# Kernel tuning notes

Measured on AMD Instinct MI355X. Metric: run time of the kernel, lower is better.

The kernel has to match this reference:

```python
import jax, jax.numpy as jnp
import numpy as np

N_USERS = 100_000
N_ENTITIES = 400_000
N_NODES = N_USERS + N_ENTITIES  # 500k
DIM = 64
N_EDGES = 2_000_000
BATCH = 4096
N_LAYERS = 3
CF_WEIGHT = 1.0
L2_REG = 1e-4


def setup_inputs() -> dict:
    key = jax.random.key(0)
    k_emb, k_e, k_u, k_p, k_n = jax.random.split(key, 5)
    # xavier_uniform on (N, D): bound = sqrt(6/(N+D))
    bound = float(np.sqrt(6.0 / (N_NODES + DIM)))
    emb = jax.random.uniform(k_emb, (N_NODES, DIM), jnp.float32, -bound, bound)
    edge_index = jax.random.randint(k_e, (2, N_EDGES), 0, N_NODES, dtype=jnp.int32)
    user_idx = jax.random.randint(k_u, (BATCH,), 0, N_USERS, dtype=jnp.int32)
    pos_item = jax.random.randint(k_p, (BATCH,), 0, N_NODES, dtype=jnp.int32)
    neg_item = jax.random.randint(k_n, (BATCH,), 0, N_NODES, dtype=jnp.int32)
    return {"emb": emb, "edge_index": edge_index, "user_idx": user_idx,
            "pos_item": pos_item, "neg_item": neg_item}


def _lightgcn(emb, edge_index, n_layers):
    # LGConv(normalize=True): x' = D^{-1/2} A D^{-1/2} x, no self loops.
    n = emb.shape[0]
    src, dst = edge_index[0], edge_index[1]
    deg = jax.ops.segment_sum(jnp.ones_like(dst, dtype=emb.dtype), dst,
                              num_segments=n)
    dinv = jnp.where(deg > 0, jax.lax.rsqrt(jnp.maximum(deg, 1e-12)), 0.0)
    norm = dinv[src] * dinv[dst]  # [E]
    x = emb
    acc = emb  # layer-0 term of the mean over stacked layers
    for _ in range(n_layers):
        msgs = x[src] * norm[:, None]  # [E, D] gather + scale
        x = jax.ops.segment_sum(msgs, dst, num_segments=n)  # scatter-add
        acc = acc + x
    return acc / (n_layers + 1)  # mean over (layers+1) stacked embeddings


def reference(emb, edge_index, user_idx, pos_item, neg_item):
    all_layer = _lightgcn(emb, edge_index, N_LAYERS)
    u = all_layer[user_idx]
    p = all_layer[pos_item]
    n_ = all_layer[neg_item]
    pos_score = jnp.sum(u * p, axis=-1)
    neg_score = jnp.sum(u * n_, axis=-1)
    # BPRLoss: -mean(logsigmoid(pos - neg)) == mean(softplus(neg - pos))
    cf_loss = jnp.mean(jax.nn.softplus(neg_score - pos_score))
    u_ego = emb[user_idx]
    p_ego = emb[pos_item]
    n_ego = emb[neg_item]
    reg_loss = 0.5 * (jnp.sum(u_ego ** 2) + jnp.sum(p_ego ** 2)
                      + jnp.sum(n_ego ** 2)) / float(BATCH)
    return CF_WEIGHT * cf_loss + L2_REG * reg_loss
```

## Files before the change

### kernel.cpp

```cpp
#include <hip/hip_runtime.h>
#include <cstdint>
#include <cstddef>

#define N_USERS   100000
#define N_NODES   500000
#define DIM       64
#define N_EDGES   2000000
#define BATCH     4096
#define SCAN_B    1024
#define NBLK      ((N_NODES + SCAN_B - 1) / SCAN_B)
#define X1C_CAP   350000
#define LA_CAP    150000
#define EDG4_BLK  ((N_EDGES / 4 + 255) / 256)
#define CONV_BLK  ((N_NODES * 16 + 255) / 256)
#define PROP_BLK  2048

typedef unsigned char uchar;
typedef unsigned short ushort;
typedef unsigned int uint;

__device__ __forceinline__ ushort f2bf(float f) {
    uint u = __float_as_uint(f);
    uint r = u + 0x7FFFu + ((u >> 16) & 1u);
    return (ushort)(r >> 16);
}
__device__ __forceinline__ float bflo(uint u) { return __uint_as_float(u << 16); }
__device__ __forceinline__ float bfhi(uint u) { return __uint_as_float(u & 0xFFFF0000u); }

__global__ void k_mark(const int* __restrict__ u, const int* __restrict__ p,
                       const int* __restrict__ n, uchar* __restrict__ f3,
                       uchar* __restrict__ fA, uchar* __restrict__ fB) {
    int i = blockIdx.x * blockDim.x + threadIdx.x;
    if (i >= 3 * BATCH) return;
    int idx;
    if (i < BATCH)          idx = u[i];
    else if (i < 2 * BATCH) idx = p[i - BATCH];
    else                    idx = n[i - 2 * BATCH];
    f3[idx] = 1; fA[idx] = 1; fB[idx] = 1;
}

__global__ void k_degconv(const int* __restrict__ src, const int* __restrict__ dst,
                          int* __restrict__ deg, const uchar* __restrict__ f3,
                          uchar* __restrict__ fA,
                          const float* __restrict__ emb, ushort* __restrict__ embs) {
    if (blockIdx.x < EDG4_BLK) {
        int t = blockIdx.x * blockDim.x + threadIdx.x;
        if (t < N_EDGES / 4) {
            int4 s0 = ((const int4*)src)[t];
            int4 d0 = ((const int4*)dst)[t];
            atomicAdd(&deg[d0.x], 1); atomicAdd(&deg[d0.y], 1);
            atomicAdd(&deg[d0.z], 1); atomicAdd(&deg[d0.w], 1);
            if (f3[d0.x] && !fA[s0.x]) fA[s0.x] = 1;
            if (f3[d0.y] && !fA[s0.y]) fA[s0.y] = 1;
            if (f3[d0.z] && !fA[s0.z]) fA[s0.z] = 1;
            if (f3[d0.w] && !fA[s0.w]) fA[s0.w] = 1;
        }
    } else {
        int c = (blockIdx.x - EDG4_BLK) * blockDim.x + threadIdx.x;
        if (c < N_NODES * 16) {
            float4 v = ((const float4*)emb)[c];
            uint2 o;
            o.x = (uint)f2bf(v.x) | ((uint)f2bf(v.y) << 16);
            o.y = (uint)f2bf(v.z) | ((uint)f2bf(v.w) << 16);
            ((uint2*)embs)[c] = o;
        }
    }
}

__global__ void k_expand(const int* __restrict__ src, const int* __restrict__ dst,
                         const uchar* __restrict__ fin, uchar* __restrict__ fout) {
    int t = blockIdx.x * blockDim.x + threadIdx.x;
    if (t < N_EDGES / 4) {
        int4 s0 = ((const int4*)src)[t];
        int4 d0 = ((const int4*)dst)[t];
        if (fin[d0.x] && !fout[s0.x]) fout[s0.x] = 1;
        if (fin[d0.y] && !fout[s0.y]) fout[s0.y] = 1;
        if (fin[d0.z] && !fout[s0.z]) fout[s0.z] = 1;
        if (fin[d0.w] && !fout[s0.w]) fout[s0.w] = 1;
    }
}

__global__ void k_scanA(const int* __restrict__ deg, const uchar* __restrict__ fA,
                        const uchar* __restrict__ fB, int* __restrict__ bsumD,
                        int* __restrict__ bsumP) {
    __shared__ int sD[SCAN_B];
    __shared__ int sP[SCAN_B];
    int i = blockIdx.x * SCAN_B + threadIdx.x;
    int d = 0, pk = 0;
    if (i < N_NODES) { d = deg[i]; pk = (int)fA[i] | ((int)fB[i] << 16); }
    sD[threadIdx.x] = d; sP[threadIdx.x] = pk;
    __syncthreads();
    for (int off = SCAN_B / 2; off; off >>= 1) {
        if (threadIdx.x < off) {
            sD[threadIdx.x] += sD[threadIdx.x + off];
            sP[threadIdx.x] += sP[threadIdx.x + off];
        }
        __syncthreads();
    }
    if (threadIdx.x == 0) { bsumD[blockIdx.x] = sD[0]; bsumP[blockIdx.x] = sP[0]; }
}

__global__ void k_scanB(const int* __restrict__ bsumD, const int* __restrict__ bsumP,
                        int* __restrict__ boffD, int* __restrict__ boffA,
                        int* __restrict__ boffB, int* __restrict__ counts) {
    __shared__ int sD[512];
    __shared__ int sA[512];
    __shared__ int sB[512];
    int d = (threadIdx.x < NBLK) ? bsumD[threadIdx.x] : 0;
    int p = (threadIdx.x < NBLK) ? bsumP[threadIdx.x] : 0;
    int a = p & 0xFFFF, b = p >> 16;
    sD[threadIdx.x] = d; sA[threadIdx.x] = a; sB[threadIdx.x] = b;
    __syncthreads();
    for (int off = 1; off < 512; off <<= 1) {
        int tD = (threadIdx.x >= off) ? sD[threadIdx.x - off] : 0;
        int tA = (threadIdx.x >= off) ? sA[threadIdx.x - off] : 0;
        int tB = (threadIdx.x >= off) ? sB[threadIdx.x - off] : 0;
        __syncthreads();
        sD[threadIdx.x] += tD; sA[threadIdx.x] += tA; sB[threadIdx.x] += tB;
        __syncthreads();
    }
    if (threadIdx.x < NBLK) {
        boffD[threadIdx.x] = sD[threadIdx.x] - d;
        boffA[threadIdx.x] = sA[threadIdx.x] - a;
        boffB[threadIdx.x] = sB[threadIdx.x] - b;
    }
    if (threadIdx.x == 511) { counts[0] = sA[511]; counts[1] = sB[511]; }
}

__global__ void k_scanC(const int* __restrict__ deg, const uchar* __restrict__ fA,
                        const uchar* __restrict__ fB,
                        const int* __restrict__ boffD, const int* __restrict__ boffA,
                        const int* __restrict__ boffB,
                        int* __restrict__ rowstart, float* __restrict__ dinv,
                        int* __restrict__ mapA, int* __restrict__ mapB,
                        int4* __restrict__ listA4, int4* __restrict__ listB4) {
    __shared__ int sD[SCAN_B];
    __shared__ int sP[SCAN_B];
    int i = blockIdx.x * SCAN_B + threadIdx.x;
    int d = 0, a = 0, b = 0;
    if (i < N_NODES) { d = deg[i]; a = (int)fA[i]; b = (int)fB[i]; }
    sD[threadIdx.x] = d; sP[threadIdx.x] = a | (b << 16);
    __syncthreads();
    for (int off = 1; off < SCAN_B; off <<= 1) {
        int tD = (threadIdx.x >= off) ? sD[threadIdx.x - off] : 0;
        int tP = (threadIdx.x >= off) ? sP[threadIdx.x - off] : 0;
        __syncthreads();
        sD[threadIdx.x] += tD; sP[threadIdx.x] += tP;
        __syncthreads();
    }
    if (i < N_NODES) {
        int exD = sD[threadIdx.x] - d + boffD[blockIdx.x];
        int incP = sP[threadIdx.x];
        int exA = (incP & 0xFFFF) - a + boffA[blockIdx.x];
        int exB = (incP >> 16) - b + boffB[blockIdx.x];
        rowstart[i] = exD;
        float dv = (d > 0) ? rsqrtf((float)d) : 0.0f;
        dinv[i] = dv;
        mapA[i] = a ? exA : -1;
        mapB[i] = b ? exB : -1;
        int4 ent = make_int4(exD, exD + d, __float_as_int(dv), 0);
        if (a) listA4[exA] = ent;
        if (b) listB4[exB] = ent;
    }
}

__global__ void k_scatter(const int* __restrict__ src, const int* __restrict__ dst,
                          const uchar* __restrict__ fB, int* __restrict__ rowstart,
                          int* __restrict__ csr_src) {
    int t = blockIdx.x * blockDim.x + threadIdx.x;
    if (t < N_EDGES / 4) {
        int4 s0 = ((const int4*)src)[t];
        int4 d0 = ((const int4*)dst)[t];
        if (fB[d0.x]) csr_src[atomicAdd(&rowstart[d0.x], 1)] = s0.x;
        if (fB[d0.y]) csr_src[atomicAdd(&rowstart[d0.y], 1)] = s0.y;
        if (fB[d0.z]) csr_src[atomicAdd(&rowstart[d0.z], 1)] = s0.z;
        if (fB[d0.w]) csr_src[atomicAdd(&rowstart[d0.w], 1)] = s0.w;
    }
}

__global__ void k_prop1(const ushort* __restrict__ embs, const int4* __restrict__ listB4,
                        const int* __restrict__ counts, const int* __restrict__ csr_src,
                        const float* __restrict__ dinv, ushort* __restrict__ x1c) {
    int lane = threadIdx.x & 63;
    int sub = lane >> 4, q = lane & 15;
    int wv = (blockIdx.x * blockDim.x + threadIdx.x) >> 6;
    int nw = (gridDim.x * blockDim.x) >> 6;
    int cnt = counts[1];
    for (; wv < cnt; wv += nw) {
        int4 nb = listB4[wv];
        float4 acc = {0.f, 0.f, 0.f, 0.f};
        for (int i = nb.x + sub; i < nb.y; i += 4) {
            int s = csr_src[i];
            float dvs = dinv[s];
            uint2 u = *(const uint2*)(embs + (size_t)s * DIM + q * 4);
            acc.x = fmaf(bflo(u.x), dvs, acc.x);
            acc.y = fmaf(bfhi(u.x), dvs, acc.y);
            acc.z = fmaf(bflo(u.y), dvs, acc.z);
            acc.w = fmaf(bfhi(u.y), dvs, acc.w);
        }
        for (int off = 16; off <= 32; off <<= 1) {
            acc.x += __shfl_xor(acc.x, off, 64);
            acc.y += __shfl_xor(acc.y, off, 64);
            acc.z += __shfl_xor(acc.z, off, 64);
            acc.w += __shfl_xor(acc.w, off, 64);
        }
        if (sub == 0) {
            float dv = __int_as_float(nb.z);
            float d2 = dv * dv;
            uint2 o;
            o.x = (uint)f2bf(acc.x * d2) | ((uint)f2bf(acc.y * d2) << 16);
            o.y = (uint)f2bf(acc.z * d2) | ((uint)f2bf(acc.w * d2) << 16);
            *(uint2*)(x1c + (size_t)wv * DIM + q * 4) = o;
        }
    }
}

__global__ void k_prop2(const ushort* __restrict__ x1c, const int* __restrict__ mapB,
                        const int4* __restrict__ listA4, const int* __restrict__ counts,
                        const int* __restrict__ csr_src, ushort* __restrict__ x2c) {
    int lane = threadIdx.x & 63;
    int sub = lane >> 4, q = lane & 15;
    int wv = (blockIdx.x * blockDim.x + threadIdx.x) >> 6;
    int nw = (gridDim.x * blockDim.x) >> 6;
    int cnt = counts[0];
    for (; wv < cnt; wv += nw) {
        int4 nb = listA4[wv];
        float4 acc = {0.f, 0.f, 0.f, 0.f};
        for (int i = nb.x + sub; i < nb.y; i += 4) {
            int s = csr_src[i];
            int slot = mapB[s];
            uint2 u = *(const uint2*)(x1c + (size_t)slot * DIM + q * 4);
            acc.x += bflo(u.x); acc.y += bfhi(u.x);
            acc.z += bflo(u.y); acc.w += bfhi(u.y);
        }
        for (int off = 16; off <= 32; off <<= 1) {
            acc.x += __shfl_xor(acc.x, off, 64);
            acc.y += __shfl_xor(acc.y, off, 64);
            acc.z += __shfl_xor(acc.z, off, 64);
            acc.w += __shfl_xor(acc.w, off, 64);
        }
        if (sub == 0) {
            float dv = __int_as_float(nb.z);
            float d2 = dv * dv;
            uint2 o;
            o.x = (uint)f2bf(acc.x * d2) | ((uint)f2bf(acc.y * d2) << 16);
            o.y = (uint)f2bf(acc.z * d2) | ((uint)f2bf(acc.w * d2) << 16);
            *(uint2*)(x2c + (size_t)wv * DIM + q * 4) = o;
        }
    }
}

__device__ __forceinline__ float x3_row(const ushort* __restrict__ x2c,
                                        const int* __restrict__ mapA,
                                        const int* __restrict__ csr_src,
                                        const int4* __restrict__ listB4,
                                        const int* __restrict__ mapB,
                                        int t, int lane) {
    int4 nb = listB4[mapB[t]];
    float acc = 0.f;
    for (int i = nb.x; i < nb.y; ++i) {
        int s = csr_src[i];
        int slot = mapA[s];
        acc += __uint_as_float((uint)x2c[(size_t)slot * DIM + lane] << 16);
    }
    return acc * __int_as_float(nb.z);
}

__global__ void k_loss(const float* __restrict__ emb, const ushort* __restrict__ x1c,
                       const ushort* __restrict__ x2c,
                       const int* __restrict__ mapA, const int* __restrict__ mapB,
                       const int4* __restrict__ listB4, const int* __restrict__ csr_src,
                       const float* __restrict__ dinv,
                       const int* __restrict__ u, const int* __restrict__ p,
                       const int* __restrict__ n, float* __restrict__ out) {
    int lane = threadIdx.x & 63;
    int w = (blockIdx.x * blockDim.x + threadIdx.x) >> 6;
    if (w >= BATCH) return;
    int ui = u[w], pi = p[w], ni = n[w];
    float dvu = dinv[ui], dvp = dinv[pi], dvn = dinv[ni];
    float rdu = dvu > 0.f ? 1.f / dvu : 0.f;
    float rdp = dvp > 0.f ? 1.f / dvp : 0.f;
    float rdn = dvn > 0.f ? 1.f / dvn : 0.f;
    float ue = emb[(size_t)ui * DIM + lane];
    float pe = emb[(size_t)pi * DIM + lane];
    float ne = emb[(size_t)ni * DIM + lane];
    float u1 = __uint_as_float((uint)x1c[(size_t)mapB[ui] * DIM + lane] << 16) * rdu;
    float p1 = __uint_as_float((uint)x1c[(size_t)mapB[pi] * DIM + lane] << 16) * rdp;
    float n1 = __uint_as_float((uint)x1c[(size_t)mapB[ni] * DIM + lane] << 16) * rdn;
    float u2 = __uint_as_float((uint)x2c[(size_t)mapA[ui] * DIM + lane] << 16) * rdu;
    float p2 = __uint_as_float((uint)x2c[(size_t)mapA[pi] * DIM + lane] << 16) * rdp;
    float n2 = __uint_as_float((uint)x2c[(size_t)mapA[ni] * DIM + lane] << 16) * rdn;
    float u3 = x3_row(x2c, mapA, csr_src, listB4, mapB, ui, lane);
    float p3 = x3_row(x2c, mapA, csr_src, listB4, mapB, pi, lane);
    float n3 = x3_row(x2c, mapA, csr_src, listB4, mapB, ni, lane);
    float uall = 0.25f * (ue + u1 + u2 + u3);
    float pall = 0.25f * (pe + p1 + p2 + p3);
    float nall = 0.25f * (ne + n1 + n2 + n3);
    float pos = uall * pall;
    float neg = uall * nall;
    float sq  = ue * ue + pe * pe + ne * ne;
    for (int off = 32; off; off >>= 1) {
        pos += __shfl_xor(pos, off, 64);
        neg += __shfl_xor(neg, off, 64);
        sq  += __shfl_xor(sq,  off, 64);
    }
    if (lane == 0) {
        float z = neg - pos;
        float sp = fmaxf(z, 0.0f) + log1pf(expf(-fabsf(z)));
        float contrib = sp * (1.0f / BATCH) + 1e-4f * 0.5f * sq * (1.0f / BATCH);
        atomicAdd(out, contrib);
    }
}

extern "C" void kernel_launch(void* const* d_in, const int* in_sizes, int n_in,
                              void* d_out, int out_size, void* d_ws, size_t ws_size,
                              hipStream_t stream) {
    const float* emb  = (const float*)d_in[0];
    const int*   edge = (const int*)d_in[1];
    const int*   src  = edge;
    const int*   dst  = edge + N_EDGES;
    const int*   uidx = (const int*)d_in[2];
    const int*   pidx = (const int*)d_in[3];
    const int*   nidx = (const int*)d_in[4];
    float* out = (float*)d_out;

    char* w = (char*)d_ws;
    ushort* embs    = (ushort*)w;                w += (size_t)N_NODES * DIM * 2;
    ushort* x1c     = (ushort*)w;                w += (size_t)X1C_CAP * DIM * 2;
    ushort* x2c     = (ushort*)w;                w += (size_t)LA_CAP * DIM * 2;
    float*  dinv    = (float*)w;                 w += (size_t)N_NODES * 4;
    int*    rowstart= (int*)w;                   w += (size_t)N_NODES * 4;
    int*    csr_src = (int*)w;                   w += (size_t)N_EDGES * 4;
    int*    mapA    = (int*)w;                   w += (size_t)N_NODES * 4;
    int*    mapB    = (int*)w;                   w += (size_t)N_NODES * 4;
    int4*   listA4  = (int4*)w;                  w += (size_t)LA_CAP * 16;
    int4*   listB4  = (int4*)w;                  w += (size_t)X1C_CAP * 16;
    char*   zbase   = w;
    int*    deg     = (int*)w;                   w += (size_t)N_NODES * 4;
    uchar*  flags   = (uchar*)w;                 w += (size_t)3 * N_NODES;
    uchar*  f3 = flags;
    uchar*  fA = flags + N_NODES;
    uchar*  fB = flags + 2 * N_NODES;
    size_t  zbytes  = (size_t)(w - zbase);
    int*    bsumD   = (int*)w;                   w += (size_t)NBLK * 4;
    int*    boffD   = (int*)w;                   w += (size_t)NBLK * 4;
    int*    bsumP   = (int*)w;                   w += (size_t)NBLK * 4;
    int*    boffA   = (int*)w;                   w += (size_t)NBLK * 4;
    int*    boffB   = (int*)w;                   w += (size_t)NBLK * 4;
    int*    counts  = (int*)w;                   w += 16;

    hipMemsetAsync(zbase, 0, zbytes, stream);
    hipMemsetAsync(out, 0, 4, stream);

    k_mark<<<(3 * BATCH + 255) / 256, 256, 0, stream>>>(uidx, pidx, nidx, f3, fA, fB);

    k_degconv<<<EDG4_BLK + CONV_BLK, 256, 0, stream>>>(src, dst, deg, f3, fA,
                                                       emb, embs);

    k_expand<<<EDG4_BLK, 256, 0, stream>>>(src, dst, fA, fB);

    k_scanA<<<NBLK, SCAN_B, 0, stream>>>(deg, fA, fB, bsumD, bsumP);
    k_scanB<<<1, 512, 0, stream>>>(bsumD, bsumP, boffD, boffA, boffB, counts);
    k_scanC<<<NBLK, SCAN_B, 0, stream>>>(deg, fA, fB, boffD, boffA, boffB,
                                         rowstart, dinv, mapA, mapB, listA4, listB4);

    k_scatter<<<EDG4_BLK, 256, 0, stream>>>(src, dst, fB, rowstart, csr_src);

    k_prop1<<<PROP_BLK, 256, 0, stream>>>(embs, listB4, counts, csr_src, dinv, x1c);
    k_prop2<<<PROP_BLK, 256, 0, stream>>>(x1c, mapB, listA4, counts, csr_src, x2c);

    k_loss<<<(BATCH * 64 + 255) / 256, 256, 0, stream>>>(
        emb, x1c, x2c, mapA, mapB, listB4, csr_src, dinv, uidx, pidx, nidx, out);
}
```

Before: 470.7 us.

## Privatize degree histogram per XCD and move bf16 conversion into scatter kernel

```diff
diff --git a/kernel.cpp b/kernel.cpp
--- a/kernel.cpp
+++ b/kernel.cpp
@@ -9,8 +9,9 @@
 #define BATCH     4096
 #define SCAN_B    1024
 #define NBLK      ((N_NODES + SCAN_B - 1) / SCAN_B)
-#define X1C_CAP   350000
-#define LA_CAP    150000
+#define X1C_CAP   280000
+#define LA_CAP    100000
+#define NXCD      8
 #define EDG4_BLK  ((N_EDGES / 4 + 255) / 256)
 #define CONV_BLK  ((N_NODES * 16 + 255) / 256)
 #define PROP_BLK  2048
@@ -26,6 +27,12 @@
 }
 __device__ __forceinline__ float bflo(uint u) { return __uint_as_float(u << 16); }
 __device__ __forceinline__ float bfhi(uint u) { return __uint_as_float(u & 0xFFFF0000u); }
+
+__device__ __forceinline__ uint xcc_id() {
+    uint x;
+    asm volatile("s_getreg_b32 %0, hwreg(HW_REG_XCC_ID)" : "=s"(x));
+    return x & (NXCD - 1);
+}
 
 __global__ void k_mark(const int* __restrict__ u, const int* __restrict__ p,
                        const int* __restrict__ n, uchar* __restrict__ f3,
@@ -39,31 +46,22 @@
     f3[idx] = 1; fA[idx] = 1; fB[idx] = 1;
 }
 
-__global__ void k_degconv(const int* __restrict__ src, const int* __restrict__ dst,
-                          int* __restrict__ deg, const uchar* __restrict__ f3,
-                          uchar* __restrict__ fA,
-                          const float* __restrict__ emb, ushort* __restrict__ embs) {
-    if (blockIdx.x < EDG4_BLK) {
-        int t = blockIdx.x * blockDim.x + threadIdx.x;
-        if (t < N_EDGES / 4) {
-            int4 s0 = ((const int4*)src)[t];
-            int4 d0 = ((const int4*)dst)[t];
-            atomicAdd(&deg[d0.x], 1); atomicAdd(&deg[d0.y], 1);
-            atomicAdd(&deg[d0.z], 1); atomicAdd(&deg[d0.w], 1);
-            if (f3[d0.x] && !fA[s0.x]) fA[s0.x] = 1;
-            if (f3[d0.y] && !fA[s0.y]) fA[s0.y] = 1;
-            if (f3[d0.z] && !fA[s0.z]) fA[s0.z] = 1;
-            if (f3[d0.w] && !fA[s0.w]) fA[s0.w] = 1;
-        }
-    } else {
-        int c = (blockIdx.x - EDG4_BLK) * blockDim.x + threadIdx.x;
-        if (c < N_NODES * 16) {
-            float4 v = ((const float4*)emb)[c];
-            uint2 o;
-            o.x = (uint)f2bf(v.x) | ((uint)f2bf(v.y) << 16);
-            o.y = (uint)f2bf(v.z) | ((uint)f2bf(v.w) << 16);
-            ((uint2*)embs)[c] = o;
-        }
+__global__ void k_deghist(const int* __restrict__ src, const int* __restrict__ dst,
+                          int* __restrict__ degp, const uchar* __restrict__ f3,
+                          uchar* __restrict__ fA) {
+    int* mydeg = degp + (size_t)xcc_id() * N_NODES;
+    int t = blockIdx.x * blockDim.x + threadIdx.x;
+    if (t < N_EDGES / 4) {
+        int4 s0 = ((const int4*)src)[t];
+        int4 d0 = ((const int4*)dst)[t];
+        __hip_atomic_fetch_add(&mydeg[d0.x], 1, __ATOMIC_RELAXED, __HIP_MEMORY_SCOPE_WORKGROUP);
+        __hip_atomic_fetch_add(&mydeg[d0.y], 1, __ATOMIC_RELAXED, __HIP_MEMORY_SCOPE_WORKGROUP);
+        __hip_atomic_fetch_add(&mydeg[d0.z], 1, __ATOMIC_RELAXED, __HIP_MEMORY_SCOPE_WORKGROUP);
+        __hip_atomic_fetch_add(&mydeg[d0.w], 1, __ATOMIC_RELAXED, __HIP_MEMORY_SCOPE_WORKGROUP);
+        if (f3[d0.x] && !fA[s0.x]) fA[s0.x] = 1;
+        if (f3[d0.y] && !fA[s0.y]) fA[s0.y] = 1;
+        if (f3[d0.z] && !fA[s0.z]) fA[s0.z] = 1;
+        if (f3[d0.w] && !fA[s0.w]) fA[s0.w] = 1;
     }
 }
 
@@ -80,14 +78,19 @@
     }
 }
 
-__global__ void k_scanA(const int* __restrict__ deg, const uchar* __restrict__ fA,
-                        const uchar* __restrict__ fB, int* __restrict__ bsumD,
-                        int* __restrict__ bsumP) {
+__global__ void k_scanA(const int* __restrict__ degp, const uchar* __restrict__ fA,
+                        const uchar* __restrict__ fB, int* __restrict__ degsum,
+                        int* __restrict__ bsumD, int* __restrict__ bsumP) {
     __shared__ int sD[SCAN_B];
     __shared__ int sP[SCAN_B];
     int i = blockIdx.x * SCAN_B + threadIdx.x;
     int d = 0, pk = 0;
-    if (i < N_NODES) { d = deg[i]; pk = (int)fA[i] | ((int)fB[i] << 16); }
+    if (i < N_NODES) {
+        #pragma unroll
+        for (int x = 0; x < NXCD; ++x) d += degp[(size_t)x * N_NODES + i];
+        degsum[i] = d;
+        pk = (int)fA[i] | ((int)fB[i] << 16);
+    }
     sD[threadIdx.x] = d; sP[threadIdx.x] = pk;
     __syncthreads();
     for (int off = SCAN_B / 2; off; off >>= 1) {
@@ -127,7 +130,7 @@
     if (threadIdx.x == 511) { counts[0] = sA[511]; counts[1] = sB[511]; }
 }
 
-__global__ void k_scanC(const int* __restrict__ deg, const uchar* __restrict__ fA,
+__global__ void k_scanC(const int* __restrict__ degsum, const uchar* __restrict__ fA,
                         const uchar* __restrict__ fB,
                         const int* __restrict__ boffD, const int* __restrict__ boffA,
                         const int* __restrict__ boffB,
@@ -138,7 +141,7 @@
     __shared__ int sP[SCAN_B];
     int i = blockIdx.x * SCAN_B + threadIdx.x;
     int d = 0, a = 0, b = 0;
-    if (i < N_NODES) { d = deg[i]; a = (int)fA[i]; b = (int)fB[i]; }
+    if (i < N_NODES) { d = degsum[i]; a = (int)fA[i]; b = (int)fB[i]; }
     sD[threadIdx.x] = d; sP[threadIdx.x] = a | (b << 16);
     __syncthreads();
     for (int off = 1; off < SCAN_B; off <<= 1) {
@@ -164,17 +167,29 @@
     }
 }
 
-__global__ void k_scatter(const int* __restrict__ src, const int* __restrict__ dst,
-                          const uchar* __restrict__ fB, int* __restrict__ rowstart,
-                          int* __restrict__ csr_src) {
-    int t = blockIdx.x * blockDim.x + threadIdx.x;
-    if (t < N_EDGES / 4) {
-        int4 s0 = ((const int4*)src)[t];
-        int4 d0 = ((const int4*)dst)[t];
-        if (fB[d0.x]) csr_src[atomicAdd(&rowstart[d0.x], 1)] = s0.x;
-        if (fB[d0.y]) csr_src[atomicAdd(&rowstart[d0.y], 1)] = s0.y;
-        if (fB[d0.z]) csr_src[atomicAdd(&rowstart[d0.z], 1)] = s0.z;
-        if (fB[d0.w]) csr_src[atomicAdd(&rowstart[d0.w], 1)] = s0.w;
+__global__ void k_convscatter(const float* __restrict__ emb, ushort* __restrict__ embs,
+                              const int* __restrict__ src, const int* __restrict__ dst,
+                              const uchar* __restrict__ fB,
+                              int* __restrict__ rowstart, int* __restrict__ csr_src) {
+    if (blockIdx.x < EDG4_BLK) {
+        int t = blockIdx.x * blockDim.x + threadIdx.x;
+        if (t < N_EDGES / 4) {
+            int4 s0 = ((const int4*)src)[t];
+            int4 d0 = ((const int4*)dst)[t];
+            if (fB[d0.x]) csr_src[atomicAdd(&rowstart[d0.x], 1)] = s0.x;
+            if (fB[d0.y]) csr_src[atomicAdd(&rowstart[d0.y], 1)] = s0.y;
+            if (fB[d0.z]) csr_src[atomicAdd(&rowstart[d0.z], 1)] = s0.z;
+            if (fB[d0.w]) csr_src[atomicAdd(&rowstart[d0.w], 1)] = s0.w;
+        }
+    } else {
+        int c = (blockIdx.x - EDG4_BLK) * blockDim.x + threadIdx.x;
+        if (c < N_NODES * 16) {
+            float4 v = ((const float4*)emb)[c];
+            uint2 o;
+            o.x = (uint)f2bf(v.x) | ((uint)f2bf(v.y) << 16);
+            o.y = (uint)f2bf(v.z) | ((uint)f2bf(v.w) << 16);
+            ((uint2*)embs)[c] = o;
+        }
     }
 }
 
@@ -333,10 +348,11 @@
     int*    csr_src = (int*)w;                   w += (size_t)N_EDGES * 4;
     int*    mapA    = (int*)w;                   w += (size_t)N_NODES * 4;
     int*    mapB    = (int*)w;                   w += (size_t)N_NODES * 4;
+    int*    degsum  = (int*)w;                   w += (size_t)N_NODES * 4;
     int4*   listA4  = (int4*)w;                  w += (size_t)LA_CAP * 16;
     int4*   listB4  = (int4*)w;                  w += (size_t)X1C_CAP * 16;
     char*   zbase   = w;
-    int*    deg     = (int*)w;                   w += (size_t)N_NODES * 4;
+    int*    degp    = (int*)w;                   w += (size_t)NXCD * N_NODES * 4;
     uchar*  flags   = (uchar*)w;                 w += (size_t)3 * N_NODES;
     uchar*  f3 = flags;
     uchar*  fA = flags + N_NODES;
@@ -354,17 +370,17 @@
 
     k_mark<<<(3 * BATCH + 255) / 256, 256, 0, stream>>>(uidx, pidx, nidx, f3, fA, fB);
 
-    k_degconv<<<EDG4_BLK + CONV_BLK, 256, 0, stream>>>(src, dst, deg, f3, fA,
-                                                       emb, embs);
+    k_deghist<<<EDG4_BLK, 256, 0, stream>>>(src, dst, degp, f3, fA);
 
     k_expand<<<EDG4_BLK, 256, 0, stream>>>(src, dst, fA, fB);
 
-    k_scanA<<<NBLK, SCAN_B, 0, stream>>>(deg, fA, fB, bsumD, bsumP);
+    k_scanA<<<NBLK, SCAN_B, 0, stream>>>(degp, fA, fB, degsum, bsumD, bsumP);
     k_scanB<<<1, 512, 0, stream>>>(bsumD, bsumP, boffD, boffA, boffB, counts);
-    k_scanC<<<NBLK, SCAN_B, 0, stream>>>(deg, fA, fB, boffD, boffA, boffB,
+    k_scanC<<<NBLK, SCAN_B, 0, stream>>>(degsum, fA, fB, boffD, boffA, boffB,
                                          rowstart, dinv, mapA, mapB, listA4, listB4);
 
-    k_scatter<<<EDG4_BLK, 256, 0, stream>>>(src, dst, fB, rowstart, csr_src);
+    k_convscatter<<<EDG4_BLK + CONV_BLK, 256, 0, stream>>>(
+        emb, embs, src, dst, fB, rowstart, csr_src);
 
     k_prop1<<<PROP_BLK, 256, 0, stream>>>(embs, listB4, counts, csr_src, dinv, x1c);
     k_prop2<<<PROP_BLK, 256, 0, stream>>>(x1c, mapB, listA4, counts, csr_src, x2c);
```

Result: slower. 485.0 us (+3.0%).
